# Performance work log

Measured on AMD Instinct MI355X. Metric: run time of the kernel, lower is better.

The kernel has to match this reference:

```python
import jax, jax.numpy as jnp
import numpy as np

HID = 512
HEADS = 8
DK = HID // HEADS


def setup_inputs() -> dict:
    key = jax.random.key(0)
    ks = jax.random.split(key, 11)
    B, Nq, Nk = 2, 4096, 4096
    s = 1.0 / np.sqrt(HID)
    inp = {
        "query": jax.random.normal(ks[0], (B, Nq, HID), jnp.float32),
        "key": jax.random.normal(ks[1], (B, Nk, HID), jnp.float32),
        "value": jax.random.normal(ks[2], (B, Nk, HID), jnp.float32),
        "Wq": jax.random.normal(ks[3], (HID, HID), jnp.float32) * s,
        "bq": jnp.zeros((HID,), jnp.float32),
        "Wk": jax.random.normal(ks[4], (HID, HID), jnp.float32) * s,
        "bk": jnp.zeros((HID,), jnp.float32),
        "Wv": jax.random.normal(ks[5], (HID, HID), jnp.float32) * s,
        "bv": jnp.zeros((HID,), jnp.float32),
        "Wo": jax.random.normal(ks[6], (HID, HID), jnp.float32) * s,
        "bo": jnp.zeros((HID,), jnp.float32),
    }
    return inp


def reference(query, key, value, Wq, bq, Wk, bk, Wv, bv, Wo, bo):
    B, Nq, _ = query.shape
    Nk = key.shape[1]
    # torch Linear: x @ W.T + b
    Q = (query @ Wq.T + bq).reshape(B, Nq, HEADS, DK).transpose(0, 2, 1, 3)  # (B,H,Nq,dk)
    K = (key @ Wk.T + bk).reshape(B, Nk, HEADS, DK).transpose(0, 2, 1, 3)    # (B,H,Nk,dk)
    V = (value @ Wv.T + bv).reshape(B, Nk, HEADS, DK).transpose(0, 2, 1, 3)  # (B,H,Nk,dk)
    scale = 1.0 / jnp.sqrt(jnp.asarray(DK, query.dtype))
    scores = jnp.einsum("bhqd,bhkd->bhqk", Q, K) * scale  # (B,H,Nq,Nk)
    attn = jax.nn.softmax(scores, axis=-1)
    # dropout is identity in eval/inference mode (deterministic reference)
    context = jnp.einsum("bhqk,bhkd->bhqd", attn, V)  # (B,H,Nq,dk)
    context = context.transpose(0, 2, 1, 3).reshape(B, Nq, HID)
    out = context @ Wo.T + bo
    return out, attn
```

## Files before the change

kernel.cpp:

```cpp
#include <hip/hip_runtime.h>
#include <hip/hip_bf16.h>

#define NB   2
#define NH   8
#define NSEQ 4096
#define DKH  64
#define HD   512

typedef unsigned short u16;
typedef unsigned int   u32;
typedef short s16x8 __attribute__((ext_vector_type(8)));
typedef u16   u16x8 __attribute__((ext_vector_type(8)));
typedef u16   u16x4 __attribute__((ext_vector_type(4)));
typedef u32   u32x2 __attribute__((ext_vector_type(2)));
typedef float f32x4 __attribute__((ext_vector_type(4)));

#define L2E 1.4426950408889634f

static __device__ __forceinline__ u16 f2bf(float f) {
    u32 u = __builtin_bit_cast(u32, f);
    u32 r = (u + 0x7fffu + ((u >> 16) & 1u)) >> 16;
    return (u16)r;
}
static __device__ __forceinline__ f32x4 mm16(s16x8 a, s16x8 b, f32x4 c) {
    return __builtin_amdgcn_mfma_f32_16x16x32_bf16(a, b, c, 0, 0, 0);
}
static __device__ __forceinline__ s16x8 ld8(const u16* p) {
    return __builtin_bit_cast(s16x8, *(const u16x8*)p);
}
static __device__ __forceinline__ void bar_sync() {
    __builtin_amdgcn_sched_barrier(0);
    asm volatile("s_waitcnt lgkmcnt(0)" ::: "memory");
    __builtin_amdgcn_sched_barrier(0);
    __builtin_amdgcn_s_barrier();
    __builtin_amdgcn_sched_barrier(0);
}

__launch_bounds__(512, 2)
__global__ void qkv_proj_kernel(const float* __restrict__ Xq, const float* __restrict__ Xk,
                                const float* __restrict__ Xv,
                                const float* __restrict__ Wq, const float* __restrict__ Wk,
                                const float* __restrict__ Wv,
                                const float* __restrict__ bq, const float* __restrict__ bk,
                                const float* __restrict__ bv,
                                u16* __restrict__ Yq, u16* __restrict__ Yk,
                                u16* __restrict__ Yv)
{
    __shared__ u16 xh[128][40], wh[128][40];
    __shared__ u16 st[9216];
    const int t = threadIdx.x;
    const int lane = t & 63, wave = t >> 6;
    const int lg = lane >> 4, lr = lane & 15;
    const int wr = (wave >> 2) * 64, wc = (wave & 3) * 32;
    const int m0 = blockIdx.x * 128, n0 = blockIdx.y * 128;

    const float* X; const float* W; const float* B; u16* Y; float scale; int mode;
    if (blockIdx.z == 0)      { X = Xq; W = Wq; B = bq; Y = Yq; scale = 0.125f * L2E; mode = 0; }
    else if (blockIdx.z == 1) { X = Xk; W = Wk; B = bk; Y = Yk; scale = 1.0f;         mode = 0; }
    else                      { X = Xv; W = Wv; B = bv; Y = Yv; scale = 1.0f;         mode = 1; }

    f32x4 acc[4][2] = {};

    for (int k0 = 0; k0 < HD; k0 += 32) {
        #pragma unroll
        for (int i = 0; i < 2; i++) {
            int idx = t + i * 512;
            int r = idx >> 3, c = (idx & 7) * 4;
            float4 v = *(const float4*)(X + (size_t)(m0 + r) * HD + k0 + c);
            u16x4 hv; hv[0] = f2bf(v.x); hv[1] = f2bf(v.y); hv[2] = f2bf(v.z); hv[3] = f2bf(v.w);
            *(u16x4*)&xh[r][c] = hv;
            float4 w = *(const float4*)(W + (size_t)(n0 + r) * HD + k0 + c);
            u16x4 gv; gv[0] = f2bf(w.x); gv[1] = f2bf(w.y); gv[2] = f2bf(w.z); gv[3] = f2bf(w.w);
            *(u16x4*)&wh[r][c] = gv;
        }
        __syncthreads();
        const int kk = lg * 8;
        s16x8 ah[4], bh[2];
        #pragma unroll
        for (int f = 0; f < 4; f++) ah[f] = ld8(&xh[wr + f * 16 + lr][kk]);
        #pragma unroll
        for (int f = 0; f < 2; f++) bh[f] = ld8(&wh[wc + f * 16 + lr][kk]);
        #pragma unroll
        for (int m = 0; m < 4; m++)
            #pragma unroll
            for (int n = 0; n < 2; n++)
                acc[m][n] = mm16(ah[m], bh[n], acc[m][n]);
        __syncthreads();
    }

    float bv2[2];
    #pragma unroll
    for (int n = 0; n < 2; n++) bv2[n] = B[n0 + wc + n * 16 + lr];

    const int mych = (wave & 3) >> 1;
    const int wcl  = wc & 63;

    #pragma unroll
    for (int ch = 0; ch < 2; ch++) {
        if (mych == ch) {
            #pragma unroll
            for (int m = 0; m < 4; m++)
                #pragma unroll
                for (int n = 0; n < 2; n++) {
                    int c = wcl + n * 16 + lr;
                    #pragma unroll
                    for (int j = 0; j < 4; j++) {
                        int r = wr + m * 16 + lg * 4 + j;
                        u16 hv = f2bf((acc[m][n][j] + bv2[n]) * scale);
                        if (mode == 0) st[r * 72 + c]  = hv;
                        else           st[c * 136 + r] = hv;
                    }
                }
        }
        __syncthreads();
        const int hh = (n0 >> 6) + ch;
        if (mode == 0) {
            #pragma unroll
            for (int i = 0; i < 2; i++) {
                int flat = t + i * 512;
                int r = flat >> 3, dc = (flat & 7) * 8;
                int row = m0 + r, b = row >> 12, nn = row & (NSEQ - 1);
                size_t o = (((size_t)(b * NH + hh) * NSEQ) + nn) * DKH + dc;
                *(u16x8*)(Y + o) = *(const u16x8*)&st[r * 72 + dc];
            }
        } else {
            #pragma unroll
            for (int i = 0; i < 2; i++) {
                int flat = t + i * 512;
                int c = flat >> 4, rc = (flat & 15) * 8;
                int row = m0 + rc, b = row >> 12, nn = row & (NSEQ - 1);
                size_t o = ((size_t)(b * NH + hh) * DKH + c) * (size_t)NSEQ + nn;
                *(u16x8*)(Y + o) = *(const u16x8*)&st[c * 136 + rc];
            }
        }
        if (ch == 0) __syncthreads();
    }
}

static __device__ __forceinline__ void swz_bh_q(int& bh, int& qblk) {
    int f = blockIdx.x + 32 * blockIdx.y;
    int r = f & 7, q = f >> 3;
    bh = 2 * r + (q >> 5);
    qblk = q & 31;
}

#define NT (NSEQ / 64)
#define PP 68

__launch_bounds__(256, 3)
__global__ void attn_kernel(const u16* __restrict__ Qh, const u16* __restrict__ Kh,
                            const u16* __restrict__ Vt,
                            float* __restrict__ attn, u16* __restrict__ ctx)
{
    __shared__ u16 kh[2][64][72], vt[2][64][72];
    __shared__ u16 plds[4][32][PP];
    const int t = threadIdx.x, lane = t & 63, wave = t >> 6;
    const int lg = lane >> 4, lr = lane & 15;
    int bh, qblk; swz_bh_q(bh, qblk);
    const int q0 = qblk * 128 + wave * 32;
    const size_t nbase = (size_t)bh * NSEQ;

    const int sr = t >> 3;
    const int sc = (t & 7) * 8;
    const u16* gK = Kh + nbase * DKH + (size_t)sr * DKH + sc;
    const u16* gV = Vt + ((size_t)bh * DKH + sr) * NSEQ + sc;

    s16x8 qh[2][2];
    #pragma unroll
    for (int qi = 0; qi < 2; qi++)
        #pragma unroll
        for (int ds = 0; ds < 2; ds++)
            qh[qi][ds] = ld8(Qh + (nbase + q0 + qi * 16 + lr) * DKH + ds * 32 + lg * 8);

    float sums[2] = {0.f, 0.f};
    {
        *(u16x8*)&kh[0][sr][sc]      = *(const u16x8*)(gK);
        *(u16x8*)&kh[0][sr + 32][sc] = *(const u16x8*)(gK + (size_t)32 * DKH);
        bar_sync();
        for (int tt = 0; tt < NT; tt++) {
            const int cur = tt & 1, nxt = cur ^ 1;
            u16x8 pk0, pk1;
            if (tt + 1 < NT) {
                pk0 = *(const u16x8*)(gK + (size_t)(tt * 64 + 64) * DKH);
                pk1 = *(const u16x8*)(gK + (size_t)(tt * 64 + 96) * DKH);
            }
            f32x4 S[2][4] = {};
            __builtin_amdgcn_s_setprio(1);
            #pragma unroll
            for (int ds = 0; ds < 2; ds++) {
                s16x8 bf[4];
                #pragma unroll
                for (int kf = 0; kf < 4; kf++)
                    bf[kf] = ld8(&kh[cur][kf * 16 + lr][ds * 32 + lg * 8]);
                #pragma unroll
                for (int qi = 0; qi < 2; qi++)
                    #pragma unroll
                    for (int kf = 0; kf < 4; kf++)
                        S[qi][kf] = mm16(bf[kf], qh[qi][ds], S[qi][kf]);
            }
            __builtin_amdgcn_s_setprio(0);
            #pragma unroll
            for (int qi = 0; qi < 2; qi++)
                #pragma unroll
                for (int kf = 0; kf < 4; kf++)
                    #pragma unroll
                    for (int j = 0; j < 4; j++)
                        sums[qi] += __builtin_amdgcn_exp2f(S[qi][kf][j]);
            if (tt + 1 < NT) {
                *(u16x8*)&kh[nxt][sr][sc]      = pk0;
                *(u16x8*)&kh[nxt][sr + 32][sc] = pk1;
            }
            bar_sync();
        }
    }
    #pragma unroll
    for (int qi = 0; qi < 2; qi++) {
        sums[qi] += __shfl_xor(sums[qi], 16, 64);
        sums[qi] += __shfl_xor(sums[qi], 32, 64);
    }

    float lrl[2];
    float* aptr[2];
    #pragma unroll
    for (int qi = 0; qi < 2; qi++) {
        lrl[qi] = -__builtin_amdgcn_logf(sums[qi]);
        aptr[qi] = attn + (nbase + q0 + qi * 16 + lr) * (size_t)NSEQ + lg * 4;
    }

    #pragma unroll
    for (int i = 0; i < 2; i++) {
        int r = sr + i * 32;
        *(u16x8*)&kh[0][r][sc] = *(const u16x8*)(gK + (size_t)(i * 32) * DKH);
        *(u16x8*)&vt[0][r][sc] = *(const u16x8*)(gV + (size_t)(i * 32) * NSEQ);
    }
    bar_sync();

    f32x4 O[2][4] = {};
    for (int tt = 0; tt < NT; tt++) {
        const int cur = tt & 1, nxt = cur ^ 1;
        const int k0 = tt * 64;

        u16x8 pk[2], pv[2];
        if (tt + 1 < NT) {
            #pragma unroll
            for (int i = 0; i < 2; i++) {
                pk[i] = *(const u16x8*)(gK + (size_t)(k0 + 64 + i * 32) * DKH);
                pv[i] = *(const u16x8*)(gV + (size_t)(i * 32) * NSEQ + k0 + 64);
            }
        }

        f32x4 S[2][4] = {};
        __builtin_amdgcn_s_setprio(1);
        #pragma unroll
        for (int ds = 0; ds < 2; ds++) {
            s16x8 bkh[4];
            #pragma unroll
            for (int kf = 0; kf < 4; kf++)
                bkh[kf] = ld8(&kh[cur][kf * 16 + lr][ds * 32 + lg * 8]);
            #pragma unroll
            for (int qi = 0; qi < 2; qi++)
                #pragma unroll
                for (int kf = 0; kf < 4; kf++)
                    S[qi][kf] = mm16(bkh[kf], qh[qi][ds], S[qi][kf]);
        }
        __builtin_amdgcn_s_setprio(0);

        #pragma unroll
        for (int qi = 0; qi < 2; qi++)
            #pragma unroll
            for (int kf = 0; kf < 4; kf++) {
                f32x4 p;
                #pragma unroll
                for (int j = 0; j < 4; j++)
                    p[j] = __builtin_amdgcn_exp2f(S[qi][kf][j] + lrl[qi]);
                *(f32x4*)(aptr[qi] + kf * 16) = p;
                u32x2 pk2;
                pk2[0] = (u32)f2bf(p[0]) | ((u32)f2bf(p[1]) << 16);
                pk2[1] = (u32)f2bf(p[2]) | ((u32)f2bf(p[3]) << 16);
                *(u32x2*)&plds[wave][qi * 16 + lr][kf * 16 + lg * 4] = pk2;
            }

        __builtin_amdgcn_wave_barrier();

        __builtin_amdgcn_s_setprio(1);
        #pragma unroll
        for (int ks = 0; ks < 2; ks++) {
            s16x8 pa[2], vb[4];
            #pragma unroll
            for (int qi = 0; qi < 2; qi++)
                pa[qi] = ld8(&plds[wave][qi * 16 + lr][ks * 32 + lg * 8]);
            #pragma unroll
            for (int df = 0; df < 4; df++)
                vb[df] = ld8(&vt[cur][df * 16 + lr][ks * 32 + lg * 8]);
            #pragma unroll
            for (int qi = 0; qi < 2; qi++)
                #pragma unroll
                for (int df = 0; df < 4; df++)
                    O[qi][df] = mm16(pa[qi], vb[df], O[qi][df]);
        }
        __builtin_amdgcn_s_setprio(0);

        if (tt + 1 < NT) {
            #pragma unroll
            for (int i = 0; i < 2; i++) {
                int r = sr + i * 32;
                *(u16x8*)&kh[nxt][r][sc] = pk[i];
                *(u16x8*)&vt[nxt][r][sc] = pv[i];
            }
        }
        aptr[0] += 64;
        aptr[1] += 64;
        bar_sync();
    }

    const int b = bh >> 3, h = bh & 7;
    #pragma unroll
    for (int qi = 0; qi < 2; qi++)
        #pragma unroll
        for (int df = 0; df < 4; df++)
            #pragma unroll
            for (int j = 0; j < 4; j++) {
                int n = q0 + qi * 16 + lg * 4 + j;
                int col = h * 64 + df * 16 + lr;
                ctx[((size_t)b * NSEQ + n) * HD + col] = f2bf(O[qi][df][j]);
            }
}

__launch_bounds__(512, 2)
__global__ void outproj_kernel(const u16* __restrict__ Xc, const float* __restrict__ W,
                               const float* __restrict__ bias, float* __restrict__ out)
{
    __shared__ u16 xh[128][72], wh[128][72];
    const int t = threadIdx.x, lane = t & 63, wave = t >> 6;
    const int lg = lane >> 4, lr = lane & 15;
    const int wr = (wave >> 2) * 64, wc = (wave & 3) * 32;
    const int m0 = blockIdx.x * 128, n0 = blockIdx.y * 128;

    f32x4 acc[4][2] = {};
    for (int k0 = 0; k0 < HD; k0 += 64) {
        #pragma unroll
        for (int i = 0; i < 2; i++) {
            int idx = t + i * 512;
            int r = idx >> 3, c = (idx & 7) * 8;
            *(u16x8*)&xh[r][c] = *(const u16x8*)(Xc + (size_t)(m0 + r) * HD + k0 + c);
        }
        #pragma unroll
        for (int i = 0; i < 4; i++) {
            int idx = t + i * 512;
            int r = idx >> 4, c = (idx & 15) * 4;
            float4 v = *(const float4*)(W + (size_t)(n0 + r) * HD + k0 + c);
            u16x4 gv; gv[0] = f2bf(v.x); gv[1] = f2bf(v.y); gv[2] = f2bf(v.z); gv[3] = f2bf(v.w);
            *(u16x4*)&wh[r][c] = gv;
        }
        __syncthreads();
        #pragma unroll
        for (int ks = 0; ks < 2; ks++) {
            s16x8 af[4], bf[2];
            int kk = ks * 32 + lg * 8;
            #pragma unroll
            for (int f = 0; f < 4; f++) af[f] = ld8(&xh[wr + f * 16 + lr][kk]);
            #pragma unroll
            for (int f = 0; f < 2; f++) bf[f] = ld8(&wh[wc + f * 16 + lr][kk]);
            #pragma unroll
            for (int m = 0; m < 4; m++)
                #pragma unroll
                for (int n = 0; n < 2; n++)
                    acc[m][n] = mm16(af[m], bf[n], acc[m][n]);
        }
        __syncthreads();
    }
    #pragma unroll
    for (int m = 0; m < 4; m++)
        #pragma unroll
        for (int n = 0; n < 2; n++) {
            int col = n0 + wc + n * 16 + lr;
            float bv = bias[col];
            #pragma unroll
            for (int j = 0; j < 4; j++) {
                int row = m0 + wr + m * 16 + lg * 4 + j;
                out[(size_t)row * HD + col] = acc[m][n][j] + bv;
            }
        }
}

extern "C" void kernel_launch(void* const* d_in, const int* in_sizes, int n_in,
                              void* d_out, int out_size, void* d_ws, size_t ws_size,
                              hipStream_t stream)
{
    const float* query = (const float*)d_in[0];
    const float* key   = (const float*)d_in[1];
    const float* value = (const float*)d_in[2];
    const float* Wq = (const float*)d_in[3];
    const float* bq = (const float*)d_in[4];
    const float* Wk = (const float*)d_in[5];
    const float* bk = (const float*)d_in[6];
    const float* Wv = (const float*)d_in[7];
    const float* bv = (const float*)d_in[8];
    const float* Wo = (const float*)d_in[9];
    const float* bo = (const float*)d_in[10];

    float* out  = (float*)d_out;
    float* attn = out + (size_t)NB * NSEQ * HD;

    const size_t E = (size_t)NB * NH * NSEQ * DKH;
    u16* qhi = (u16*)d_ws;
    u16* khi = qhi + E;
    u16* vt  = khi + E;
    u16* ctx = vt + E;

    qkv_proj_kernel<<<dim3(64, 4, 3), dim3(512), 0, stream>>>(
        query, key, value, Wq, Wk, Wv, bq, bk, bv, qhi, khi, vt);
    attn_kernel<<<dim3(32, 16), dim3(256), 0, stream>>>(qhi, khi, vt, attn, ctx);
    outproj_kernel<<<dim3(64, 4), dim3(512), 0, stream>>>(ctx, Wo, bo, out);
}
```

Baseline: 387.3 us.

## Load K/V MFMA fragments directly from global memory, dropping LDS staging

The attention kernel no longer stages K and V tiles through double-buffered shared memory. Each wave loads its MFMA operand fragments straight from global (L2-cached) memory, which removes the block-wide barriers and LDS traffic. The cost is that each of the 4 waves reads the same K/V data separately, so global and L2 load traffic rises fourfold, and there is no explicit prefetch to hide load latency. The variable name contains a non-ASCII character, which may or may not compile.

After: 552.3 us. 1.43x slower.

```diff
diff --git a/kernel.cpp b/kernel.cpp
--- a/kernel.cpp
+++ b/kernel.cpp
@@ -27,13 +27,6 @@
 }
 static __device__ __forceinline__ s16x8 ld8(const u16* p) {
     return __builtin_bit_cast(s16x8, *(const u16x8*)p);
-}
-static __device__ __forceinline__ void bar_sync() {
-    __builtin_amdgcn_sched_barrier(0);
-    asm volatile("s_waitcnt lgkmcnt(0)" ::: "memory");
-    __builtin_amdgcn_sched_barrier(0);
-    __builtin_amdgcn_s_barrier();
-    __builtin_amdgcn_sched_barrier(0);
 }
 
 __launch_bounds__(512, 2)
@@ -152,7 +145,6 @@
                             const u16* __restrict__ Vt,
                             float* __restrict__ attn, u16* __restrict__ ctx)
 {
-    __shared__ u16 kh[2][64][72], vt[2][64][72];
     __shared__ u16 plds[4][32][PP];
     const int t = threadIdx.x, lane = t & 63, wave = t >> 6;
     const int lg = lane >> 4, lr = lane & 15;
@@ -160,10 +152,8 @@
     const int q0 = qblk * 128 + wave * 32;
     const size_t nbase = (size_t)bh * NSEQ;
 
-    const int sr = t >> 3;
-    const int sc = (t & 7) * 8;
-    const u16* gK = Kh + nbase * DKH + (size_t)sr * DKH + sc;
-    const u16* gV = Vt + ((size_t)bh * DKH + sr) * NSEQ + sc;
+    const u16* kfrag = Kh + (nbase + lr) * DKH + lg * 8;
+    const u16* vfrag = Vt + ((size_t)bh * DKH + lr) * NSEQ + lg * 8;
 
     s16x8 qh[2][2];
     #pragma unroll
@@ -173,45 +163,31 @@
             qh[qi][ds] = ld8(Qh + (nbase + q0 + qi * 16 + lr) * DKH + ds * 32 + lg * 8);
 
     float sums[2] = {0.f, 0.f};
-    {
-        *(u16x8*)&kh[0][sr][sc]      = *(const u16x8*)(gK);
-        *(u16x8*)&kh[0][sr + 32][sc] = *(const u16x8*)(gK + (size_t)32 * DKH);
-        bar_sync();
-        for (int tt = 0; tt < NT; tt++) {
-            const int cur = tt & 1, nxt = cur ^ 1;
-            u16x8 pk0, pk1;
-            if (tt + 1 < NT) {
-                pk0 = *(const u16x8*)(gK + (size_t)(tt * 64 + 64) * DKH);
-                pk1 = *(const u16x8*)(gK + (size_t)(tt * 64 + 96) * DKH);
-            }
-            f32x4 S[2][4] = {};
-            __builtin_amdgcn_s_setprio(1);
-            #pragma unroll
-            for (int ds = 0; ds < 2; ds++) {
-                s16x8 bf[4];
+    for (int tt = 0; tt < NT; tt++) {
+        const size_t kو = (size_t)tt * 64 * DKH;
+        s16x8 bf[2][4];
+        #pragma unroll
+        for (int ds = 0; ds < 2; ds++)
+            #pragma unroll
+            for (int kf = 0; kf < 4; kf++)
+                bf[ds][kf] = ld8(kfrag + kو + (size_t)kf * 16 * DKH + ds * 32);
+        f32x4 S[2][4] = {};
+        __builtin_amdgcn_s_setprio(1);
+        #pragma unroll
+        for (int ds = 0; ds < 2; ds++)
+            #pragma unroll
+            for (int qi = 0; qi < 2; qi++)
                 #pragma unroll
                 for (int kf = 0; kf < 4; kf++)
-                    bf[kf] = ld8(&kh[cur][kf * 16 + lr][ds * 32 + lg * 8]);
-                #pragma unroll
-                for (int qi = 0; qi < 2; qi++)
-                    #pragma unroll
-                    for (int kf = 0; kf < 4; kf++)
-                        S[qi][kf] = mm16(bf[kf], qh[qi][ds], S[qi][kf]);
-            }
-            __builtin_amdgcn_s_setprio(0);
-            #pragma unroll
-            for (int qi = 0; qi < 2; qi++)
-                #pragma unroll
-                for (int kf = 0; kf < 4; kf++)
-                    #pragma unroll
-                    for (int j = 0; j < 4; j++)
-                        sums[qi] += __builtin_amdgcn_exp2f(S[qi][kf][j]);
-            if (tt + 1 < NT) {
-                *(u16x8*)&kh[nxt][sr][sc]      = pk0;
-                *(u16x8*)&kh[nxt][sr + 32][sc] = pk1;
-            }
-            bar_sync();
-        }
+                    S[qi][kf] = mm16(bf[ds][kf], qh[qi][ds], S[qi][kf]);
+        __builtin_amdgcn_s_setprio(0);
+        #pragma unroll
+        for (int qi = 0; qi < 2; qi++)
+            #pragma unroll
+            for (int kf = 0; kf < 4; kf++)
+                #pragma unroll
+                for (int j = 0; j < 4; j++)
+                    sums[qi] += __builtin_amdgcn_exp2f(S[qi][kf][j]);
     }
     #pragma unroll
     for (int qi = 0; qi < 2; qi++) {
@@ -227,42 +203,32 @@
         aptr[qi] = attn + (nbase + q0 + qi * 16 + lr) * (size_t)NSEQ + lg * 4;
     }
 
-    #pragma unroll
-    for (int i = 0; i < 2; i++) {
-        int r = sr + i * 32;
-        *(u16x8*)&kh[0][r][sc] = *(const u16x8*)(gK + (size_t)(i * 32) * DKH);
-        *(u16x8*)&vt[0][r][sc] = *(const u16x8*)(gV + (size_t)(i * 32) * NSEQ);
-    }
-    bar_sync();
-
     f32x4 O[2][4] = {};
     for (int tt = 0; tt < NT; tt++) {
-        const int cur = tt & 1, nxt = cur ^ 1;
         const int k0 = tt * 64;
-
-        u16x8 pk[2], pv[2];
-        if (tt + 1 < NT) {
-            #pragma unroll
-            for (int i = 0; i < 2; i++) {
-                pk[i] = *(const u16x8*)(gK + (size_t)(k0 + 64 + i * 32) * DKH);
-                pv[i] = *(const u16x8*)(gV + (size_t)(i * 32) * NSEQ + k0 + 64);
-            }
-        }
+        const size_t kو = (size_t)k0 * DKH;
+
+        s16x8 bkh[2][4], vb[2][4];
+        #pragma unroll
+        for (int ds = 0; ds < 2; ds++)
+            #pragma unroll
+            for (int kf = 0; kf < 4; kf++)
+                bkh[ds][kf] = ld8(kfrag + kو + (size_t)kf * 16 * DKH + ds * 32);
+        #pragma unroll
+        for (int ks = 0; ks < 2; ks++)
+            #pragma unroll
+            for (int df = 0; df < 4; df++)
+                vb[ks][df] = ld8(vfrag + (size_t)df * 16 * NSEQ + k0 + ks * 32);
 
         f32x4 S[2][4] = {};
         __builtin_amdgcn_s_setprio(1);
         #pragma unroll
-        for (int ds = 0; ds < 2; ds++) {
-            s16x8 bkh[4];
-            #pragma unroll
-            for (int kf = 0; kf < 4; kf++)
-                bkh[kf] = ld8(&kh[cur][kf * 16 + lr][ds * 32 + lg * 8]);
+        for (int ds = 0; ds < 2; ds++)
             #pragma unroll
             for (int qi = 0; qi < 2; qi++)
                 #pragma unroll
                 for (int kf = 0; kf < 4; kf++)
-                    S[qi][kf] = mm16(bkh[kf], qh[qi][ds], S[qi][kf]);
-        }
+                    S[qi][kf] = mm16(bkh[ds][kf], qh[qi][ds], S[qi][kf]);
         __builtin_amdgcn_s_setprio(0);
 
         #pragma unroll
@@ -285,32 +251,20 @@
         __builtin_amdgcn_s_setprio(1);
         #pragma unroll
         for (int ks = 0; ks < 2; ks++) {
-            s16x8 pa[2], vb[4];
+            s16x8 pa[2];
             #pragma unroll
             for (int qi = 0; qi < 2; qi++)
                 pa[qi] = ld8(&plds[wave][qi * 16 + lr][ks * 32 + lg * 8]);
             #pragma unroll
-            for (int df = 0; df < 4; df++)
-                vb[df] = ld8(&vt[cur][df * 16 + lr][ks * 32 + lg * 8]);
-            #pragma unroll
             for (int qi = 0; qi < 2; qi++)
                 #pragma unroll
                 for (int df = 0; df < 4; df++)
-                    O[qi][df] = mm16(pa[qi], vb[df], O[qi][df]);
+                    O[qi][df] = mm16(pa[qi], vb[ks][df], O[qi][df]);
         }
         __builtin_amdgcn_s_setprio(0);
 
-        if (tt + 1 < NT) {
-            #pragma unroll
-            for (int i = 0; i < 2; i++) {
-                int r = sr + i * 32;
-                *(u16x8*)&kh[nxt][r][sc] = pk[i];
-                *(u16x8*)&vt[nxt][r][sc] = pv[i];
-            }
-        }
         aptr[0] += 64;
         aptr[1] += 64;
-        bar_sync();
     }
 
     const int b = bh >> 3, h = bh & 7;
```
